# Kernel tuning notes

Hardware: AMD Instinct MI355X
Metric: run time of the kernel (lower is better)

The kernel has to match this reference:

```python
import math
import jax, jax.numpy as jnp
import numpy as np

H = 12          # num_attention_heads
D = 128         # head_dim = 1536 // 12
E = H * D       # hidden_size
CHUNK = 12      # attention_chunk_size
PAST = 12       # attention_context_left - 1
FUT = 0         # attention_context_right
CTX = CHUNK + PAST + FUT   # 24
CAP = 50.0      # attention_logit_cap
Q_SCALE = D ** (-0.5) / math.log(2.0)
K_SCALE = math.log(1.0 + math.e) / math.log(2.0)


def setup_inputs() -> dict:
    key = jax.random.key(0)
    ks = jax.random.split(key, 8)
    B, S = 8, 3072
    w_scale = E ** (-0.5)
    return {
        "hidden_states": jax.random.normal(ks[0], (B, S, E), jnp.float32),
        "position_embeddings": jax.random.normal(ks[1], (CTX, E), jnp.float32),
        "w_q": jax.random.normal(ks[2], (E, E), jnp.float32) * w_scale,
        "w_k": jax.random.normal(ks[3], (E, E), jnp.float32) * w_scale,
        "w_v": jax.random.normal(ks[4], (E, E), jnp.float32) * w_scale,
        "w_post": jax.random.normal(ks[5], (E, E), jnp.float32) * w_scale,
        "w_rel": jax.random.normal(ks[6], (E, E), jnp.float32) * w_scale,
        "per_dim_scale": jnp.zeros((D,), jnp.float32),
    }


def _rel_shift(x):
    # x: [B, H, nb, chunk, P] with P <= CTX+1 -> [B, H, nb, chunk, CTX]
    B, h, nb, bs, p = x.shape
    x = jnp.pad(x, ((0, 0), (0, 0), (0, 0), (0, 0), (0, CTX + 1 - p)))
    x = x.reshape(B, h, nb, bs * (CTX + 1))[..., : bs * CTX]
    return x.reshape(B, h, nb, bs, CTX)


def reference(hidden_states, position_embeddings, w_q, w_k, w_v, w_post, w_rel, per_dim_scale):
    B, S, _ = hidden_states.shape
    # projections (torch Linear: y = x @ W.T), computed in float32
    q = (hidden_states @ w_q.T).reshape(B, S, H, D)
    k = (hidden_states @ w_k.T).reshape(B, S, H, D)
    v = (hidden_states @ w_v.T).reshape(B, S, H, D)
    q = q * (Q_SCALE * jax.nn.softplus(per_dim_scale))  # per-dim query scale
    k = k * K_SCALE

    nb = (S + CHUNK - 1) // CHUNK
    pad = nb * CHUNK - S
    # convert_to_block: [B, nb, CHUNK, H, D]
    qb = jnp.pad(q, ((0, 0), (0, pad), (0, 0), (0, 0))).reshape(B, nb, CHUNK, H, D)

    def ctx_extract(x):
        # pad left by PAST, right by FUT + CHUNK - 1, then gather CTX-wide windows strided by CHUNK
        xp = jnp.pad(x, ((0, 0), (PAST, FUT + CHUNK - 1), (0, 0), (0, 0)))
        idx = jnp.arange(nb)[:, None] * CHUNK + jnp.arange(CTX)[None, :]
        return xp[:, idx]  # [B, nb, CTX, H, D]

    kc = ctx_extract(k)
    vc = ctx_extract(v)

    rel_k = (position_embeddings @ w_rel.T).reshape(-1, H, D)  # [P, H, D]

    # content term: [B, H, nb, CHUNK, CTX]
    ac = jnp.einsum('bnchd,bnkhd->bhnck', qb, kc)
    # position term + Transformer-XL rel shift
    bd = jnp.einsum('bnchd,phd->bhncp', qb, rel_k)
    bd = _rel_shift(bd)

    logits = ac + bd
    logits = jnp.tanh(logits / CAP) * CAP  # softcap
    attn_weights = jax.nn.softmax(logits, axis=-1)

    out = jnp.einsum('bhnck,bnkhd->bnchd', attn_weights, vc)
    out = out.reshape(B, nb * CHUNK, H * D)[:, :S]
    out = out @ w_post.T
    return out, attn_weights
```

## Files before the change

kernel.cpp:

```cpp
#include <hip/hip_runtime.h>
#include <hip/hip_bf16.h>

#define HH 12
#define DD 128
#define EE 1536
#define QKVP 4608
#define NBATCH 8
#define SEQ 3072
#define NBLK 256
#define CHK 12
#define CTXW 24
#define MTOK 24576

#define Q_SCALE_BASE 0.12751743f
#define K_SCALE_F 1.8946361322f

typedef short s16x8 __attribute__((ext_vector_type(8)));
typedef float f32x4 __attribute__((ext_vector_type(4)));

__device__ __forceinline__ float bf2f(unsigned short u) {
  return __builtin_bit_cast(float, ((unsigned int)u) << 16);
}
__device__ __forceinline__ unsigned short f2bf(float f) {
  unsigned int u = __builtin_bit_cast(unsigned int, f);
  u += 0x7fffu + ((u >> 16) & 1u);
  return (unsigned short)(u >> 16);
}
__device__ __forceinline__ void bf2f2(unsigned int u, float& lo, float& hi) {
  lo = __builtin_bit_cast(float, u << 16);
  hi = __builtin_bit_cast(float, u & 0xffff0000u);
}

__device__ __forceinline__ void async16(const void* g, void* l) {
  __builtin_amdgcn_global_load_lds(
      (const __attribute__((address_space(1))) unsigned int*)g,
      (__attribute__((address_space(3))) unsigned int*)l, 16, 0, 0);
}

__global__ __launch_bounds__(256) void k_cvt(const float4* __restrict__ in,
                                             ushort4* __restrict__ out, int n4) {
  int i = blockIdx.x * 256 + threadIdx.x;
  if (i < n4) {
    float4 v = in[i];
    ushort4 o;
    o.x = f2bf(v.x); o.y = f2bf(v.y); o.z = f2bf(v.z); o.w = f2bf(v.w);
    out[i] = o;
  }
}

__global__ void k_qscale(const float* __restrict__ pds, float* __restrict__ qs) {
  int d = threadIdx.x;
  if (d < DD) {
    float x = pds[d];
    float sp = (x > 20.f) ? x : log1pf(expf(x));
    qs[d] = Q_SCALE_BASE * sp;
  }
}

__global__ __launch_bounds__(256) void k_rel(const float* __restrict__ pos,
                                             const float* __restrict__ w_rel,
                                             unsigned short* __restrict__ rel16) {
  __shared__ unsigned short lp[12 * EE];
  const int t = threadIdx.x;
  const int p0 = blockIdx.y * 12;
  for (int i = t; i < 12 * EE / 4; i += 256) {
    float4 x = ((const float4*)(pos + (long)p0 * EE))[i];
    ushort4 o; o.x = f2bf(x.x); o.y = f2bf(x.y); o.z = f2bf(x.z); o.w = f2bf(x.w);
    ((ushort4*)lp)[i] = o;
  }
  __syncthreads();
  const int col = blockIdx.x * 128 + (t & 127);
  const int pg = t >> 7;
  float acc[6] = {0.f, 0.f, 0.f, 0.f, 0.f, 0.f};
  const float* wr = w_rel + (long)col * EE;
  for (int e = 0; e < EE; e += 4) {
    float4 w4 = *(const float4*)&wr[e];
#pragma unroll
    for (int i = 0; i < 6; ++i) {
      const unsigned short* lpr = &lp[(pg * 6 + i) * EE + e];
      unsigned int u01 = *(const unsigned int*)lpr;
      unsigned int u23 = *(const unsigned int*)(lpr + 2);
      float a0, a1, a2, a3;
      bf2f2(u01, a0, a1); bf2f2(u23, a2, a3);
      acc[i] += w4.x * a0 + w4.y * a1 + w4.z * a2 + w4.w * a3;
    }
  }
#pragma unroll
  for (int i = 0; i < 6; ++i)
    rel16[(long)(p0 + pg * 6 + i) * EE + col] = f2bf(acc[i]);
}


__device__ __forceinline__ void stage_half(const unsigned short* g0, long Kl,
                                           unsigned short* lhalf,
                                           int w, int rlo, int qz) {
  const unsigned short* s0 = g0 + (long)(w * 16 + rlo) * Kl + qz * 8;
  async16(s0,          lhalf + w * 1024);
  async16(s0 + 8 * Kl, lhalf + w * 1024 + 512);
}

__device__ __forceinline__ void tile4(
    unsigned short* AP, unsigned short* BP,
    unsigned short* AQ, unsigned short* BQ,
    const unsigned short* gAt, const unsigned short* gBt, long Kl,
    int t1, int t2, int w, int rlo, int qz,
    int aBase, int bBase, int sw0, int sw1, f32x4 (&acc)[8][4]) {
  s16x8 af[4], bf[4];

#pragma unroll
  for (int i = 0; i < 4; ++i) af[i] = *(const s16x8*)&AP[(aBase + 16 * i) * 64 + sw0];
#pragma unroll
  for (int j = 0; j < 4; ++j) bf[j] = *(const s16x8*)&BP[(bBase + 16 * j) * 64 + sw0];
  stage_half(gAt + (long)t1 * 64, Kl, AQ, w, rlo, qz);
  __builtin_amdgcn_s_barrier();
  __builtin_amdgcn_s_setprio(1);
#pragma unroll
  for (int i = 0; i < 4; ++i)
#pragma unroll
    for (int j = 0; j < 4; ++j)
      acc[i][j] = __builtin_amdgcn_mfma_f32_16x16x32_bf16(af[i], bf[j], acc[i][j], 0, 0, 0);
  __builtin_amdgcn_s_setprio(0);
  __builtin_amdgcn_s_barrier();

#pragma unroll
  for (int i = 0; i < 4; ++i) af[i] = *(const s16x8*)&AP[(aBase + 64 + 16 * i) * 64 + sw0];
  stage_half(gAt + 128 * Kl + (long)t1 * 64, Kl, AQ + 8192, w, rlo, qz);
  __builtin_amdgcn_s_barrier();
  __builtin_amdgcn_s_setprio(1);
#pragma unroll
  for (int i = 0; i < 4; ++i)
#pragma unroll
    for (int j = 0; j < 4; ++j)
      acc[4 + i][j] = __builtin_amdgcn_mfma_f32_16x16x32_bf16(af[i], bf[j], acc[4 + i][j], 0, 0, 0);
  __builtin_amdgcn_s_setprio(0);
  __builtin_amdgcn_s_barrier();

#pragma unroll
  for (int i = 0; i < 4; ++i) af[i] = *(const s16x8*)&AP[(aBase + 16 * i) * 64 + sw1];
#pragma unroll
  for (int j = 0; j < 4; ++j) bf[j] = *(const s16x8*)&BP[(bBase + 16 * j) * 64 + sw1];
  __builtin_amdgcn_s_barrier();
  __builtin_amdgcn_s_setprio(1);
#pragma unroll
  for (int i = 0; i < 4; ++i)
#pragma unroll
    for (int j = 0; j < 4; ++j)
      acc[i][j] = __builtin_amdgcn_mfma_f32_16x16x32_bf16(af[i], bf[j], acc[i][j], 0, 0, 0);
  __builtin_amdgcn_s_setprio(0);
  __builtin_amdgcn_s_barrier();

#pragma unroll
  for (int i = 0; i < 4; ++i) af[i] = *(const s16x8*)&AP[(aBase + 64 + 16 * i) * 64 + sw1];
  stage_half(gBt + (long)t2 * 64, Kl, BP, w, rlo, qz);
  stage_half(gBt + 128 * Kl + (long)t2 * 64, Kl, BP + 8192, w, rlo, qz);
  asm volatile("s_waitcnt vmcnt(4)" ::: "memory");
  __builtin_amdgcn_s_barrier();
  __builtin_amdgcn_s_setprio(1);
#pragma unroll
  for (int i = 0; i < 4; ++i)
#pragma unroll
    for (int j = 0; j < 4; ++j)
      acc[4 + i][j] = __builtin_amdgcn_mfma_f32_16x16x32_bf16(af[i], bf[j], acc[4 + i][j], 0, 0, 0);
  __builtin_amdgcn_s_setprio(0);
  __builtin_amdgcn_s_barrier();
}

__global__ __launch_bounds__(512, 2) void k_gemm256(
    const unsigned short* __restrict__ A, const unsigned short* __restrict__ Bt,
    void* __restrict__ Cv, int M, int N, int K, int gN,
    int mode, const float* __restrict__ qscale, int c_f32) {
  __shared__ unsigned short sm[65536];

  const int tid = threadIdx.x;
  const int w = tid >> 6;
  const int lane = tid & 63;
  const int quad = lane >> 4;
  const int l16 = lane & 15;
  const int sw = l16 & 7;
  const int rlo = lane >> 3;
  const int qz = (lane & 7) ^ rlo;

  const int nwg = gridDim.x;
  const int orig = blockIdx.x;
  const int qd = nwg >> 3;
  const int xcd = orig & 7;
  const int u = orig >> 3;
  const int bandsz = 4 * gN;
  const int band = u / bandsz;
  const int rem = u - band * bandsz;
  const int mi = band * 4 + (rem & 3);
  const int ni = rem >> 2;
  const int mloc = qd / gN;
  const int mt = xcd * mloc + mi;
  const int nt = ni;
  const long bm = (long)mt * 256, bn = (long)nt * 256;
  const long Kl = K;
  const unsigned short* gAt = A + bm * Kl;
  const unsigned short* gBt = Bt + bn * Kl;

  unsigned short* A0 = sm;
  unsigned short* B0 = sm + 16384;
  unsigned short* A1 = sm + 32768;
  unsigned short* B1 = sm + 49152;

  const int aBase = (w >> 2) * 128 + l16;
  const int bBase = (w & 3) * 64 + l16;
  const int sw0 = ((quad ^ sw) & 7) * 8;
  const int sw1 = (((4 | quad) ^ sw) & 7) * 8;

  f32x4 acc[8][4] = {};
  const int NT = K >> 6;

  stage_half(gAt,            Kl, A0,        w, rlo, qz);
  stage_half(gAt + 128 * Kl, Kl, A0 + 8192, w, rlo, qz);
  stage_half(gBt,            Kl, B0,        w, rlo, qz);
  stage_half(gBt + 128 * Kl, Kl, B0 + 8192, w, rlo, qz);
  stage_half(gBt + 64,            Kl, B1,        w, rlo, qz);
  stage_half(gBt + 128 * Kl + 64, Kl, B1 + 8192, w, rlo, qz);
  asm volatile("s_waitcnt vmcnt(4)" ::: "memory");
  __builtin_amdgcn_s_barrier();

  for (int t = 0; t < NT; t += 2) {
    const int t1 = t + 1;
    const int t2 = (t + 2 == NT) ? 0 : t + 2;
    const int t3 = (t + 3 >= NT) ? t + 3 - NT : t + 3;
    tile4(A0, B0, A1, B1, gAt, gBt, Kl, t1, t2, w, rlo, qz, aBase, bBase, sw0, sw1, acc);
    tile4(A1, B1, A0, B0, gAt, gBt, Kl, t2, t3, w, rlo, qz, aBase, bBase, sw0, sw1, acc);
  }

  __syncthreads();

  const int wmq = (w >> 2) * 128;
  const int wnq = (w & 3) * 64;

  if (!c_f32) {
#pragma unroll
    for (int j = 0; j < 4; ++j) {
      const long col = bn + wnq + 16 * j + l16;
      float scale = 1.0f;
      if (mode == 3)
        scale = (col < 1536) ? qscale[col & (DD - 1)] : (col < 3072 ? K_SCALE_F : 1.0f);
      const int lc = wnq + 16 * j + l16;
#pragma unroll
      for (int i = 0; i < 8; ++i) {
        const int lr0 = wmq + 16 * i + quad * 4;
#pragma unroll
        for (int r = 0; r < 4; ++r) {
          const int lr = lr0 + r;
          const int gsw = (lc >> 3) ^ ((lr >> 2) & 7);
          sm[lr * 256 + gsw * 8 + (lc & 7)] = f2bf(acc[i][j][r] * scale);
        }
      }
    }
    __syncthreads();
#pragma unroll
    for (int k = 0; k < 16; ++k) {
      const int G = k * 512 + tid;
      const int row = G >> 5, gc = G & 31;
      const int gsw = gc ^ ((row >> 2) & 7);
      s16x8 vdat = *(const s16x8*)&sm[row * 256 + gsw * 8];
      *(s16x8*)&((unsigned short*)Cv)[(bm + row) * (long)N + bn + gc * 8] = vdat;
    }
  } else {
    float* Cf = (float*)sm;
#pragma unroll
    for (int h = 0; h < 2; ++h) {
      if ((wmq == 0) == (h == 0)) {
#pragma unroll
        for (int j = 0; j < 4; ++j) {
          const long col = bn + wnq + 16 * j + l16;
          float scale = 1.0f;
          if (mode == 3)
            scale = (col < 1536) ? qscale[col & (DD - 1)] : (col < 3072 ? K_SCALE_F : 1.0f);
          const int lc = wnq + 16 * j + l16;
#pragma unroll
          for (int i = 0; i < 8; ++i) {
            const int lr0 = 16 * i + quad * 4;
#pragma unroll
            for (int r = 0; r < 4; ++r) {
              const int lr = lr0 + r;
              const int gsw = (lc >> 2) ^ ((lr >> 2) & 7);
              Cf[lr * 256 + gsw * 4 + (lc & 3)] = acc[i][j][r] * scale;
            }
          }
        }
      }
      __syncthreads();
#pragma unroll
      for (int k = 0; k < 16; ++k) {
        const int G = k * 512 + tid;
        const int row = G >> 6, gc = G & 63;
        const int gsw = gc ^ ((row >> 2) & 7);
        float4 vdat = *(const float4*)&Cf[row * 256 + gsw * 4];
        *(float4*)&((float*)Cv)[(bm + h * 128 + row) * (long)N + bn + gc * 4] = vdat;
      }
      __syncthreads();
    }
  }
}

__global__ __launch_bounds__(256) void k_attn(
    const unsigned short* __restrict__ qkv, const unsigned short* __restrict__ rel,
    unsigned short* __restrict__ attn_out, float* __restrict__ aw_out) {
  const int n = blockIdx.x;
  const int b = blockIdx.y;
  const int h = blockIdx.z;
  const int t = threadIdx.x;
  const int wv = t >> 6;
  const int lane = t & 63;
  const int quad = lane >> 4;
  const int l16 = lane & 15;

  __shared__ unsigned short lq[16 * 128];
  __shared__ unsigned short lk[32 * 128];
  __shared__ unsigned short lrel[32 * 128];
  __shared__ unsigned short lvt[128 * 40];
  __shared__ unsigned short lw[16 * 40];
  __shared__ float sac[16 * 33];
  __shared__ float sbd[16 * 33];
  __shared__ unsigned short sO[12 * 136];
  __shared__ float smax[12], sinv[12];

  const long tok0 = (long)b * SEQ + (long)n * CHK;
  const long hq = (long)h * DD;

  for (int u = t; u < 192; u += 256) {
    int r = u >> 4, w4 = u & 15;
    uint4 x = *(const uint4*)&qkv[(tok0 + r) * QKVP + hq + w4 * 8];
    *(uint4*)&lq[r * 128 + ((w4 ^ (r & 7)) * 8)] = x;
  }
  for (int u = t; u < 384; u += 256) {
    int r = u >> 4, w4 = u & 15;
    int s = n * CHK + r - 12;
    uint4 kx = make_uint4(0, 0, 0, 0);
    if (s >= 0) kx = *(const uint4*)&qkv[((long)b * SEQ + s) * QKVP + hq + 1536 + w4 * 8];
    *(uint4*)&lk[r * 128 + ((w4 ^ (r & 7)) * 8)] = kx;
    uint4 rx = *(const uint4*)&rel[(long)r * EE + hq + w4 * 8];
    *(uint4*)&lrel[r * 128 + ((w4 ^ (r & 7)) * 8)] = rx;
  }
  for (int u = t; u < 384; u += 256) {
    int r = u >> 4, d16 = u & 15, d0 = d16 * 8;
    int s = n * CHK + r - 12;
    uint4 vx = make_uint4(0, 0, 0, 0);
    if (s >= 0) vx = *(const uint4*)&qkv[((long)b * SEQ + s) * QKVP + hq + 3072 + d0];
    unsigned short vs[8];
    *(uint4*)vs = vx;
#pragma unroll
    for (int i = 0; i < 8; ++i) {
      int ii = (i + d16) & 7;
      lvt[(d0 + ii) * 40 + r] = vs[ii];
    }
  }
  for (int u = t; u < 128; u += 256)
    *(uint4*)&lvt[u * 40 + 24] = make_uint4(0, 0, 0, 0);
  for (int u = t; u < 80; u += 256)
    *(uint4*)&lw[u * 8] = make_uint4(0, 0, 0, 0);
  __syncthreads();

  {
    const unsigned short* bsrc = (wv < 2) ? lk : lrel;
    const int nt = wv & 1;
    f32x4 acc = {};
#pragma unroll
    for (int dc = 0; dc < 4; ++dc) {
      const int g = dc * 4 + quad;
      s16x8 a = *(const s16x8*)&lq[l16 * 128 + ((g ^ (l16 & 7)) * 8)];
      const int rB = nt * 16 + l16;
      s16x8 bb = *(const s16x8*)&bsrc[rB * 128 + ((g ^ (rB & 7)) * 8)];
      acc = __builtin_amdgcn_mfma_f32_16x16x32_bf16(a, bb, acc, 0, 0, 0);
    }
    float* dstp = (wv < 2) ? sac : sbd;
#pragma unroll
    for (int r = 0; r < 4; ++r)
      dstp[(quad * 4 + r) * 33 + nt * 16 + l16] = acc[r];
  }
  __syncthreads();

  for (int p = t; p < CHK * CTXW; p += 256) {
    int c = p / CTXW, j = p - c * CTXW;
    float y;
    if (j >= c) y = sbd[c * 33 + (j - c)];
    else if (j == c - 1) y = 0.f;
    else y = sbd[(c - 1) * 33 + (j - c + CTXW + 1)];
    float x = (sac[c * 33 + j] + y) * 0.02f;
    x = fminf(fmaxf(x, -15.f), 15.f);
    float e2 = __expf(2.f * x);
    sac[c * 33 + j] = 50.f * (e2 - 1.f) / (e2 + 1.f);
  }
  __syncthreads();

  if (t < CHK) {
    float m = -3.0e38f;
#pragma unroll
    for (int j = 0; j < CTXW; ++j) m = fmaxf(m, sac[t * 33 + j]);
    smax[t] = m;
  }
  __syncthreads();

  for (int p = t; p < CHK * CTXW; p += 256) {
    int c = p / CTXW, j = p - c * CTXW;
    sbd[c * 33 + j] = __expf(sac[c * 33 + j] - smax[c]);
  }
  __syncthreads();

  if (t < CHK) {
    float s = 0.f;
#pragma unroll
    for (int j = 0; j < CTXW; ++j) s += sbd[t * 33 + j];
    sinv[t] = 1.f / s;
  }
  __syncthreads();

  for (int p = t; p < CHK * CTXW; p += 256) {
    int c = p / CTXW, j = p - c * CTXW;
    float wgt = sbd[c * 33 + j] * sinv[c];
    aw_out[((((long)b * HH + h) * NBLK + n) * CHK + c) * CTXW + j] = wgt;
    lw[c * 40 + j] = f2bf(wgt);
  }
  __syncthreads();

  {
    s16x8 afw = *(const s16x8*)&lw[l16 * 40 + quad * 8];
#pragma unroll
    for (int e = 0; e < 2; ++e) {
      const int dnt = wv * 2 + e;
      s16x8 bv = *(const s16x8*)&lvt[(dnt * 16 + l16) * 40 + quad * 8];
      f32x4 o = __builtin_amdgcn_mfma_f32_16x16x32_bf16(afw, bv, (f32x4){}, 0, 0, 0);
#pragma unroll
      for (int r = 0; r < 4; ++r) {
        const int row = quad * 4 + r;
        if (row < CHK) sO[row * 136 + dnt * 16 + l16] = f2bf(o[r]);
      }
    }
  }
  __syncthreads();

  for (int u = t; u < 192; u += 256) {
    int r = u >> 4, w4 = u & 15;
    uint4 x = *(const uint4*)&sO[r * 136 + w4 * 8];
    *(uint4*)&attn_out[(tok0 + r) * EE + hq + w4 * 8] = x;
  }
}

extern "C" void kernel_launch(void* const* d_in, const int* in_sizes, int n_in,
                              void* d_out, int out_size, void* d_ws, size_t ws_size,
                              hipStream_t stream) {
  const float* hs     = (const float*)d_in[0];
  const float* pos    = (const float*)d_in[1];
  const float* w_q    = (const float*)d_in[2];
  const float* w_k    = (const float*)d_in[3];
  const float* w_v    = (const float*)d_in[4];
  const float* w_post = (const float*)d_in[5];
  const float* w_rel  = (const float*)d_in[6];
  const float* pds    = (const float*)d_in[7];

  char* ws = (char*)d_ws;
  const size_t TOKB = (size_t)MTOK * EE * 2;
  const size_t WB   = (size_t)EE * EE * 2;
  unsigned short* hs16   = (unsigned short*)(ws);
  unsigned short* qkv16  = (unsigned short*)(ws + TOKB);
  unsigned short* wq16   = (unsigned short*)(ws + 4 * TOKB);
  unsigned short* wk16   = (unsigned short*)(ws + 4 * TOKB + WB);
  unsigned short* wv16   = (unsigned short*)(ws + 4 * TOKB + 2 * WB);
  unsigned short* wp16   = (unsigned short*)(ws + 4 * TOKB + 3 * WB);
  unsigned short* rel16  = (unsigned short*)(ws + 4 * TOKB + 4 * WB);
  float* qscale          = (float*)(ws + 4 * TOKB + 4 * WB + CTXW * EE * 2);
  unsigned short* attn16 = hs16;

  float* out = (float*)d_out;
  float* aw  = out + (size_t)MTOK * EE;

  k_cvt<<<36864, 256, 0, stream>>>((const float4*)hs, (ushort4*)hs16, MTOK * EE / 4);
  k_cvt<<<2304, 256, 0, stream>>>((const float4*)w_q, (ushort4*)wq16, EE * EE / 4);
  k_cvt<<<2304, 256, 0, stream>>>((const float4*)w_k, (ushort4*)wk16, EE * EE / 4);
  k_cvt<<<2304, 256, 0, stream>>>((const float4*)w_v, (ushort4*)wv16, EE * EE / 4);
  k_cvt<<<2304, 256, 0, stream>>>((const float4*)w_post, (ushort4*)wp16, EE * EE / 4);
  k_qscale<<<1, 128, 0, stream>>>(pds, qscale);
  k_rel<<<dim3(12, 2), 256, 0, stream>>>(pos, w_rel, rel16);

  k_gemm256<<<dim3((MTOK / 256) * (QKVP / 256)), 512, 0, stream>>>(
      hs16, wq16, qkv16, MTOK, QKVP, EE, QKVP / 256, 3, qscale, 0);

  k_attn<<<dim3(NBLK, NBATCH, HH), 256, 0, stream>>>(qkv16, rel16, attn16, aw);

  k_gemm256<<<dim3((MTOK / 256) * (EE / 256)), 512, 0, stream>>>(
      attn16, wp16, out, MTOK, EE, EE, EE / 256, 0, nullptr, 1);
}
```

Measured before the change: 987.3 us.

## Process four attention chunks per block to share overlapping K/V windows

The attention kernel now handles four consecutive 12-token chunks per 512-thread block instead of one chunk per 256-thread block. It loads a 64-row K/V span and the relative-position table once and reuses them across the overlapping 24-wide context windows, so each K/V row is fetched from global memory fewer times. Content logits are computed as a banded set of MFMA tiles over a 48x64 score matrix, the transposed V layout is re-swizzled, and the P·V product becomes a 48-row matmul. In exchange the block uses about 72 KB of shared memory and more threads, which lowers how many blocks fit per CU, and some MFMA work is spent on padded tiles.

New measurement: 931.5 us. 1.06x faster.

```diff
diff --git a/kernel.cpp b/kernel.cpp
--- a/kernel.cpp
+++ b/kernel.cpp
@@ -299,10 +299,10 @@
   }
 }
 
-__global__ __launch_bounds__(256) void k_attn(
+__global__ __launch_bounds__(512, 4) void k_attn(
     const unsigned short* __restrict__ qkv, const unsigned short* __restrict__ rel,
     unsigned short* __restrict__ attn_out, float* __restrict__ aw_out) {
-  const int n = blockIdx.x;
+  const int ng = blockIdx.x;
   const int b = blockIdx.y;
   const int h = blockIdx.z;
   const int t = threadIdx.x;
@@ -311,134 +311,159 @@
   const int quad = lane >> 4;
   const int l16 = lane & 15;
 
-  __shared__ unsigned short lq[16 * 128];
-  __shared__ unsigned short lk[32 * 128];
-  __shared__ unsigned short lrel[32 * 128];
-  __shared__ unsigned short lvt[128 * 40];
-  __shared__ unsigned short lw[16 * 40];
-  __shared__ float sac[16 * 33];
-  __shared__ float sbd[16 * 33];
-  __shared__ unsigned short sO[12 * 136];
-  __shared__ float smax[12], sinv[12];
-
-  const long tok0 = (long)b * SEQ + (long)n * CHK;
+  __shared__ __align__(16) char smem[72064];
+  unsigned short* lq   = (unsigned short*)(smem);
+  unsigned short* lk   = (unsigned short*)(smem + 12288);
+  unsigned short* lrel = (unsigned short*)(smem + 28672);
+  unsigned short* lvt  = (unsigned short*)(smem + 36864);
+  float* sS  = (float*)(smem + 53248);
+  float* sBD = (float*)(smem + 65728);
+  unsigned short* lw = (unsigned short*)(smem + 12288);
+  unsigned short* sO = (unsigned short*)(smem + 18432);
+  __shared__ float smax[48], sinv[48];
+
+  const int n0 = ng * 4;
+  const long tokq0 = (long)b * SEQ + (long)n0 * CHK;
   const long hq = (long)h * DD;
 
-  for (int u = t; u < 192; u += 256) {
-    int r = u >> 4, w4 = u & 15;
-    uint4 x = *(const uint4*)&qkv[(tok0 + r) * QKVP + hq + w4 * 8];
-    *(uint4*)&lq[r * 128 + ((w4 ^ (r & 7)) * 8)] = x;
-  }
-  for (int u = t; u < 384; u += 256) {
-    int r = u >> 4, w4 = u & 15;
-    int s = n * CHK + r - 12;
-    uint4 kx = make_uint4(0, 0, 0, 0);
-    if (s >= 0) kx = *(const uint4*)&qkv[((long)b * SEQ + s) * QKVP + hq + 1536 + w4 * 8];
-    *(uint4*)&lk[r * 128 + ((w4 ^ (r & 7)) * 8)] = kx;
-    uint4 rx = *(const uint4*)&rel[(long)r * EE + hq + w4 * 8];
-    *(uint4*)&lrel[r * 128 + ((w4 ^ (r & 7)) * 8)] = rx;
-  }
-  for (int u = t; u < 384; u += 256) {
-    int r = u >> 4, d16 = u & 15, d0 = d16 * 8;
-    int s = n * CHK + r - 12;
-    uint4 vx = make_uint4(0, 0, 0, 0);
-    if (s >= 0) vx = *(const uint4*)&qkv[((long)b * SEQ + s) * QKVP + hq + 3072 + d0];
+  for (int u = t; u < 48 * 16; u += 512) {
+    int r = u >> 4, g = u & 15;
+    uint4 x = *(const uint4*)&qkv[(tokq0 + r) * QKVP + hq + g * 8];
+    *(uint4*)&lq[r * 128 + ((g ^ (r & 7)) * 8)] = x;
+  }
+  for (int u = t; u < 64 * 16; u += 512) {
+    int r = u >> 4, g = u & 15;
+    int s = n0 * CHK - 12 + r;
+    uint4 kx = make_uint4(0, 0, 0, 0), vx = make_uint4(0, 0, 0, 0);
+    if (s >= 0 && s < SEQ) {
+      const unsigned short* base = &qkv[((long)b * SEQ + s) * QKVP + hq];
+      kx = *(const uint4*)&base[1536 + g * 8];
+      vx = *(const uint4*)&base[3072 + g * 8];
+    }
+    *(uint4*)&lk[r * 128 + ((g ^ (r & 7)) * 8)] = kx;
     unsigned short vs[8];
     *(uint4*)vs = vx;
 #pragma unroll
     for (int i = 0; i < 8; ++i) {
-      int ii = (i + d16) & 7;
-      lvt[(d0 + ii) * 40 + r] = vs[ii];
-    }
-  }
-  for (int u = t; u < 128; u += 256)
-    *(uint4*)&lvt[u * 40 + 24] = make_uint4(0, 0, 0, 0);
-  for (int u = t; u < 80; u += 256)
-    *(uint4*)&lw[u * 8] = make_uint4(0, 0, 0, 0);
-  __syncthreads();
-
-  {
-    const unsigned short* bsrc = (wv < 2) ? lk : lrel;
-    const int nt = wv & 1;
-    f32x4 acc = {};
-#pragma unroll
-    for (int dc = 0; dc < 4; ++dc) {
-      const int g = dc * 4 + quad;
-      s16x8 a = *(const s16x8*)&lq[l16 * 128 + ((g ^ (l16 & 7)) * 8)];
-      const int rB = nt * 16 + l16;
-      s16x8 bb = *(const s16x8*)&bsrc[rB * 128 + ((g ^ (rB & 7)) * 8)];
-      acc = __builtin_amdgcn_mfma_f32_16x16x32_bf16(a, bb, acc, 0, 0, 0);
-    }
-    float* dstp = (wv < 2) ? sac : sbd;
-#pragma unroll
-    for (int r = 0; r < 4; ++r)
-      dstp[(quad * 4 + r) * 33 + nt * 16 + l16] = acc[r];
-  }
-  __syncthreads();
-
-  for (int p = t; p < CHK * CTXW; p += 256) {
-    int c = p / CTXW, j = p - c * CTXW;
+      int gr = (r >> 3) ^ i ^ (g & 3);
+      lvt[(g * 8 + i) * 64 + gr * 8 + (r & 7)] = vs[i];
+    }
+  }
+  for (int u = t; u < 32 * 16; u += 512) {
+    int r = u >> 4, g = u & 15;
+    uint4 rx = make_uint4(0, 0, 0, 0);
+    if (r < CTXW) rx = *(const uint4*)&rel[(long)r * EE + hq + g * 8];
+    *(uint4*)&lrel[r * 128 + ((g ^ (r & 7)) * 8)] = rx;
+  }
+  __syncthreads();
+
+  for (int pi = wv; pi < 15; pi += 8) {
+    if (pi < 9) {
+      const int mi = pi / 3;
+      const int ni = pi % 3 + (mi == 2 ? 1 : 0);
+      f32x4 c4 = {};
+#pragma unroll
+      for (int dc = 0; dc < 4; ++dc) {
+        s16x8 a  = *(const s16x8*)&lq[(mi * 16 + l16) * 128 + (((dc * 4 + quad) ^ (l16 & 7)) * 8)];
+        s16x8 bb = *(const s16x8*)&lk[(ni * 16 + l16) * 128 + (((dc * 4 + quad) ^ (l16 & 7)) * 8)];
+        c4 = __builtin_amdgcn_mfma_f32_16x16x32_bf16(a, bb, c4, 0, 0, 0);
+      }
+#pragma unroll
+      for (int r = 0; r < 4; ++r)
+        sS[(mi * 16 + quad * 4 + r) * 65 + ni * 16 + l16] = c4[r];
+    } else {
+      const int q = pi - 9;
+      const int mi = q >> 1, nj = q & 1;
+      f32x4 c4 = {};
+#pragma unroll
+      for (int dc = 0; dc < 4; ++dc) {
+        s16x8 a  = *(const s16x8*)&lq[(mi * 16 + l16) * 128 + (((dc * 4 + quad) ^ (l16 & 7)) * 8)];
+        s16x8 bb = *(const s16x8*)&lrel[(nj * 16 + l16) * 128 + (((dc * 4 + quad) ^ (l16 & 7)) * 8)];
+        c4 = __builtin_amdgcn_mfma_f32_16x16x32_bf16(a, bb, c4, 0, 0, 0);
+      }
+#pragma unroll
+      for (int r = 0; r < 4; ++r)
+        sBD[(mi * 16 + quad * 4 + r) * 33 + nj * 16 + l16] = c4[r];
+    }
+  }
+  __syncthreads();
+
+  for (int p = t; p < 48 * CTXW; p += 512) {
+    int i = p / CTXW, j = p - i * CTXW;
+    int cl = i / 12, r = i - cl * 12;
     float y;
-    if (j >= c) y = sbd[c * 33 + (j - c)];
-    else if (j == c - 1) y = 0.f;
-    else y = sbd[(c - 1) * 33 + (j - c + CTXW + 1)];
-    float x = (sac[c * 33 + j] + y) * 0.02f;
+    if (j >= r) y = sBD[i * 33 + (j - r)];
+    else if (j == r - 1) y = 0.f;
+    else y = sBD[(i - 1) * 33 + (j - r + CTXW + 1)];
+    int jj = cl * 12 + j;
+    float x = (sS[i * 65 + jj] + y) * 0.02f;
     x = fminf(fmaxf(x, -15.f), 15.f);
     float e2 = __expf(2.f * x);
-    sac[c * 33 + j] = 50.f * (e2 - 1.f) / (e2 + 1.f);
-  }
-  __syncthreads();
-
-  if (t < CHK) {
+    sS[i * 65 + jj] = 50.f * (e2 - 1.f) / (e2 + 1.f);
+  }
+  __syncthreads();
+
+  if (t < 48) {
+    int base = t * 65 + (t / 12) * 12;
     float m = -3.0e38f;
 #pragma unroll
-    for (int j = 0; j < CTXW; ++j) m = fmaxf(m, sac[t * 33 + j]);
+    for (int j = 0; j < CTXW; ++j) m = fmaxf(m, sS[base + j]);
     smax[t] = m;
   }
   __syncthreads();
 
-  for (int p = t; p < CHK * CTXW; p += 256) {
-    int c = p / CTXW, j = p - c * CTXW;
-    sbd[c * 33 + j] = __expf(sac[c * 33 + j] - smax[c]);
-  }
-  __syncthreads();
-
-  if (t < CHK) {
+  for (int p = t; p < 48 * CTXW; p += 512) {
+    int i = p / CTXW, j = p - i * CTXW;
+    int jj = (i / 12) * 12 + j;
+    sS[i * 65 + jj] = __expf(sS[i * 65 + jj] - smax[i]);
+  }
+  __syncthreads();
+
+  if (t < 48) {
+    int base = t * 65 + (t / 12) * 12;
     float s = 0.f;
 #pragma unroll
-    for (int j = 0; j < CTXW; ++j) s += sbd[t * 33 + j];
+    for (int j = 0; j < CTXW; ++j) s += sS[base + j];
     sinv[t] = 1.f / s;
   }
   __syncthreads();
 
-  for (int p = t; p < CHK * CTXW; p += 256) {
-    int c = p / CTXW, j = p - c * CTXW;
-    float wgt = sbd[c * 33 + j] * sinv[c];
-    aw_out[((((long)b * HH + h) * NBLK + n) * CHK + c) * CTXW + j] = wgt;
-    lw[c * 40 + j] = f2bf(wgt);
+  for (int p = t; p < 48 * 64; p += 512) {
+    int i = p >> 6, jj = p & 63;
+    int cl = i / 12;
+    int j = jj - cl * 12;
+    float wgt = 0.f;
+    if (j >= 0 && j < CTXW) {
+      wgt = sS[i * 65 + jj] * sinv[i];
+      aw_out[((((long)b * HH + h) * NBLK + (n0 + cl)) * CHK + (i - cl * 12)) * CTXW + j] = wgt;
+    }
+    lw[i * 64 + (((jj >> 3) ^ (i & 7)) * 8) + (jj & 7)] = f2bf(wgt);
   }
   __syncthreads();
 
   {
-    s16x8 afw = *(const s16x8*)&lw[l16 * 40 + quad * 8];
-#pragma unroll
-    for (int e = 0; e < 2; ++e) {
-      const int dnt = wv * 2 + e;
-      s16x8 bv = *(const s16x8*)&lvt[(dnt * 16 + l16) * 40 + quad * 8];
-      f32x4 o = __builtin_amdgcn_mfma_f32_16x16x32_bf16(afw, bv, (f32x4){}, 0, 0, 0);
-#pragma unroll
-      for (int r = 0; r < 4; ++r) {
-        const int row = quad * 4 + r;
-        if (row < CHK) sO[row * 136 + dnt * 16 + l16] = f2bf(o[r]);
+    const int rowv = wv * 16 + l16;
+    const int vx3 = (rowv >> 3) & 3;
+#pragma unroll
+    for (int mi = 0; mi < 3; ++mi) {
+      f32x4 o4 = {};
+#pragma unroll
+      for (int ks = 0; ks < 2; ++ks) {
+        s16x8 a  = *(const s16x8*)&lw[(mi * 16 + l16) * 64 + (((ks * 4 + quad) ^ (l16 & 7)) * 8)];
+        s16x8 bb = *(const s16x8*)&lvt[rowv * 64 + ((((ks * 4 + quad) ^ (l16 & 7)) ^ vx3) * 8)];
+        o4 = __builtin_amdgcn_mfma_f32_16x16x32_bf16(a, bb, o4, 0, 0, 0);
       }
-    }
-  }
-  __syncthreads();
-
-  for (int u = t; u < 192; u += 256) {
-    int r = u >> 4, w4 = u & 15;
-    uint4 x = *(const uint4*)&sO[r * 136 + w4 * 8];
-    *(uint4*)&attn_out[(tok0 + r) * EE + hq + w4 * 8] = x;
+#pragma unroll
+      for (int r = 0; r < 4; ++r)
+        sO[(mi * 16 + quad * 4 + r) * 136 + wv * 16 + l16] = f2bf(o4[r]);
+    }
+  }
+  __syncthreads();
+
+  for (int u = t; u < 48 * 16; u += 512) {
+    int r = u >> 4, g = u & 15;
+    uint4 x = *(const uint4*)&sO[r * 136 + g * 8];
+    *(uint4*)&attn_out[(tokq0 + r) * EE + hq + g * 8] = x;
   }
 }
 
@@ -481,7 +506,7 @@
   k_gemm256<<<dim3((MTOK / 256) * (QKVP / 256)), 512, 0, stream>>>(
       hs16, wq16, qkv16, MTOK, QKVP, EE, QKVP / 256, 3, qscale, 0);
 
-  k_attn<<<dim3(NBLK, NBATCH, HH), 256, 0, stream>>>(qkv16, rel16, attn16, aw);
+  k_attn<<<dim3(NBLK / 4, NBATCH, HH), 512, 0, stream>>>(qkv16, rel16, attn16, aw);
 
   k_gemm256<<<dim3((MTOK / 256) * (EE / 256)), 512, 0, stream>>>(
       attn16, wp16, out, MTOK, EE, EE, EE / 256, 0, nullptr, 1);
```
